# Kernel optimization log

Measured on AMD Instinct MI355X. Metric: run time of the kernel, lower is better.

## Reference

```python
import jax, jax.numpy as jnp
import numpy as np

NUM_SEG = 533  # ~ 400*400/300 superpixels from SLIC
C_FEAT = 2112
H = W = 400
SIM_THRESH = 0.97


def setup_inputs() -> dict:
    key = jax.random.key(0)
    ks = jax.random.split(key, 8)
    inp = {
        "feature_maps": jax.random.normal(ks[0], (C_FEAT, H, W), jnp.float32),
        "sp": jax.random.randint(ks[1], (H, W), 0, NUM_SEG, jnp.int32),
        "y": jax.random.randint(ks[2], (H, W), 0, 3, jnp.int32),
        "w1": jax.random.normal(ks[3], (C_FEAT, 1024), jnp.float32) * 0.02,
        "b1": jnp.zeros((1024,), jnp.float32),
        "w2": jax.random.normal(ks[4], (1024, 1024), jnp.float32) * 0.02,
        "b2": jnp.zeros((1024,), jnp.float32),
        "w3": jax.random.normal(ks[5], (1024, 32), jnp.float32) * 0.02,
        "b3": jnp.zeros((32,), jnp.float32),
        "wc": jax.random.normal(ks[6], (32, 2), jnp.float32) * 0.02,
        "bc": jnp.zeros((2,), jnp.float32),
    }
    return inp


def reference(feature_maps, sp, y, w1, b1, w2, b2, w3, b3, wc, bc):
    C = feature_maps.shape[0]
    feats = feature_maps.reshape(C, -1).T            # [HW, C]
    seg = sp.reshape(-1)                             # [HW]

    # fused per-superpixel gather + mean (replaces the per-segment Python loop)
    sums = jax.ops.segment_sum(feats, seg, num_segments=NUM_SEG)          # [S, C]
    cnts = jax.ops.segment_sum(jnp.ones_like(seg, dtype=feats.dtype), seg,
                               num_segments=NUM_SEG)                      # [S]
    mean_feat = sums / jnp.maximum(cnts, 1.0)[:, None]                    # [S, C]

    # per-superpixel majority label over classes {0,1,2}
    onehot = jax.nn.one_hot(y.reshape(-1), 3, dtype=jnp.float32)          # [HW, 3]
    counts = jax.ops.segment_sum(onehot, seg, num_segments=NUM_SEG)       # [S, 3]
    lab = jnp.argmax(counts, axis=1)                                      # first max, like torch
    ones_c, twos_c = counts[:, 1], counts[:, 2]
    tie_break = jnp.where(twos_c > ones_c, 2, jnp.where(ones_c > twos_c, 1, 0))
    lab = jnp.where(lab == 0, tie_break, lab)                             # [S]

    # batched MLP + classifier (replaces per-segment calls)
    h = jax.nn.relu(mean_feat @ w1 + b1)
    h = jax.nn.relu(h @ w2 + b2)
    h = jax.nn.relu(h @ w3 + b3)
    preds = jax.nn.softmax(h @ wc + bc, axis=-1)                          # [S, 2]

    # cosine-similarity kNN label propagation (matmul form of the O(n*m) loop)
    labeled = lab != 0
    det = jax.lax.stop_gradient(mean_feat)
    nrm = det / jnp.maximum(jnp.linalg.norm(det, axis=1, keepdims=True), 1e-12)
    aff = nrm @ nrm.T                                                     # [S, S]
    aff_masked = jnp.where(labeled[None, :], aff, -jnp.inf)               # cols: labeled only
    best = jnp.max(aff_masked, axis=1)
    best_idx = jnp.argmax(aff_masked, axis=1)
    propagate = (~labeled) & (best >= SIM_THRESH)
    new_lab = jnp.where(propagate, lab[best_idx], lab)                    # [S]

    return preds, lab, labeled, new_lab
```

## Files before the change

kernel.cpp:

```cpp
#include <hip/hip_runtime.h>
#include <math.h>

#define NSEG 533
#define CFEAT 2112
#define PIX 160000
#define SIM_THRESH 0.97f
#define RPG 1250
#define NCG 33
#define RTOT (RPG * NCG)
#define NBLK 256

typedef __attribute__((ext_vector_type(4))) float f32x4;
typedef __attribute__((ext_vector_type(4))) int   i32x4;
typedef __attribute__((ext_vector_type(8))) short bf16x8;

__device__ inline unsigned short f2bf_u16(float f) {
    unsigned u = __builtin_bit_cast(unsigned, f);
    return (unsigned short)((u + 0x7FFFu + ((u >> 16) & 1u)) >> 16);
}

__global__ __launch_bounds__(256) void k_counts(const int* __restrict__ sp,
                                                const int* __restrict__ y,
                                                int* __restrict__ c3) {
    __shared__ int h[NSEG * 3];
    for (int e = threadIdx.x; e < NSEG * 3; e += 256) h[e] = 0;
    __syncthreads();
    const int base = blockIdx.x * 5000;
    for (int p = threadIdx.x; p < 5000; p += 256) {
        int idx = base + p;
        atomicAdd(&h[sp[idx] * 3 + y[idx]], 1);
    }
    __syncthreads();
    for (int e = threadIdx.x; e < NSEG * 3; e += 256) {
        int v = h[e];
        if (v) atomicAdd(&c3[e], v);
    }
}

__global__ __launch_bounds__(256) void k_labels(const int* __restrict__ c3,
                                                int* __restrict__ lab,
                                                float* __restrict__ invc,
                                                float* __restrict__ out) {
    int s = blockIdx.x * 256 + threadIdx.x;
    if (s >= NSEG) return;
    int c0 = c3[s * 3 + 0], c1 = c3[s * 3 + 1], c2 = c3[s * 3 + 2];
    int cnt = c0 + c1 + c2;
    int idx = 0, best = c0;
    if (c1 > best) { best = c1; idx = 1; }
    if (c2 > best) { best = c2; idx = 2; }
    if (idx == 0) idx = (c2 > c1) ? 2 : ((c1 > c2) ? 1 : 0);
    lab[s] = idx;
    invc[s] = 1.0f / (float)(cnt > 0 ? cnt : 1);
    out[1066 + s] = (float)idx;
    out[1599 + s] = (idx != 0) ? 1.0f : 0.0f;
}

__global__ __launch_bounds__(1024, 4) void k_segsum_mfma(const float* __restrict__ fm,
                                                         const int* __restrict__ sp,
                                                         float* __restrict__ sums) {
    __shared__ char Bs[2][64 * 128];
    const int tid = threadIdx.x;
    const int lane = tid & 63, wave = tid >> 6;
    const int r = lane & 15, kg = lane >> 4;
    const int nmt = (wave < 2) ? 3 : 2;
    const int rswz = (r & 7) << 3;
    const int sch = tid >> 4;
    const int spx = tid & 15;
    const int wswz = (sch & 7) << 3;

    long long t0 = ((long long)blockIdx.x * RTOT) / NBLK;
    const long long t1 = ((long long)(blockIdx.x + 1) * RTOT) / NBLK;

    while (t0 < t1) {
        const int cg = (int)(t0 / RPG);
        const int r0 = (int)(t0 - (long long)cg * RPG);
        const long long cgend = (long long)(cg + 1) * RPG;
        const int rend = (int)(((t1 < cgend) ? t1 : cgend) - (long long)cg * RPG);
        const int c0 = cg * 64;
        const float* fmg = fm + (size_t)(c0 + sch) * PIX + spx * 8;

        f32x4 acc[3][4] = {};

        auto stage = [&](int rr) {
            const float* src = fmg + rr * 128;
            f32x4 u0 = *(const f32x4*)src;
            f32x4 u1 = *(const f32x4*)(src + 4);
            int w0 = __builtin_amdgcn_cvt_pk_fp8_f32(u0[0], u0[1], 0, false);
            w0 = __builtin_amdgcn_cvt_pk_fp8_f32(u0[2], u0[3], w0, true);
            int w1 = __builtin_amdgcn_cvt_pk_fp8_f32(u1[0], u1[1], 0, false);
            w1 = __builtin_amdgcn_cvt_pk_fp8_f32(u1[2], u1[3], w1, true);
            uint2 w = { (unsigned)w0, (unsigned)w1 };
            *(uint2*)(Bs[rr & 1] + sch * 128 + ((spx * 8) ^ wswz)) = w;
        };

        stage(r0);
        __syncthreads();

        for (int rr = r0; rr < rend; ++rr) {
            const bool pf = (rr + 1 < rend);
            f32x4 u0 = {}, u1 = {};
            if (pf) {
                const float* src = fmg + (rr + 1) * 128;
                u0 = *(const f32x4*)src;
                u1 = *(const f32x4*)(src + 4);
            }
            const char* bufc = Bs[rr & 1];
            const int* spr = sp + rr * 128 + kg * 8;
            i32x4 sa = *(const i32x4*)spr;
            i32x4 sb = *(const i32x4*)(spr + 4);

            #pragma unroll
            for (int ks = 0; ks < 4; ++ks) {
                i32x4 na, nb;
                if (ks < 3) {
                    na = *(const i32x4*)(spr + (ks + 1) * 32);
                    nb = *(const i32x4*)(spr + (ks + 1) * 32 + 4);
                }
                int seg[8] = { sa[0], sa[1], sa[2], sa[3], sb[0], sb[1], sb[2], sb[3] };
                uint2 vb[4];
                #pragma unroll
                for (int nt = 0; nt < 4; ++nt)
                    vb[nt] = *(const uint2*)(bufc + (nt * 16 + r) * 128 +
                                             ((ks * 32 + kg * 8) ^ rswz));
                #pragma unroll
                for (int i = 0; i < 3; ++i) {
                    if (i < nmt) {
                        const int tm = (i < 2) ? wave * 2 + i : 32 + wave;
                        const int tgt = tm * 16 + r;
                        unsigned a0 = ((seg[0] == tgt) ? 0x38u : 0u) |
                                      ((seg[1] == tgt) ? 0x3800u : 0u) |
                                      ((seg[2] == tgt) ? 0x380000u : 0u) |
                                      ((seg[3] == tgt) ? 0x38000000u : 0u);
                        unsigned a1 = ((seg[4] == tgt) ? 0x38u : 0u) |
                                      ((seg[5] == tgt) ? 0x3800u : 0u) |
                                      ((seg[6] == tgt) ? 0x380000u : 0u) |
                                      ((seg[7] == tgt) ? 0x3800u * 0x10000u : 0u);
                        if (__any((a0 | a1) != 0u)) {
                            long long av = __builtin_bit_cast(long long, (uint2){ a0, a1 });
                            acc[i][0] = __builtin_amdgcn_mfma_f32_16x16x32_fp8_fp8(
                                av, __builtin_bit_cast(long long, vb[0]), acc[i][0], 0, 0, 0);
                            acc[i][1] = __builtin_amdgcn_mfma_f32_16x16x32_fp8_fp8(
                                av, __builtin_bit_cast(long long, vb[1]), acc[i][1], 0, 0, 0);
                            acc[i][2] = __builtin_amdgcn_mfma_f32_16x16x32_fp8_fp8(
                                av, __builtin_bit_cast(long long, vb[2]), acc[i][2], 0, 0, 0);
                            acc[i][3] = __builtin_amdgcn_mfma_f32_16x16x32_fp8_fp8(
                                av, __builtin_bit_cast(long long, vb[3]), acc[i][3], 0, 0, 0);
                        }
                    }
                }
                if (ks < 3) { sa = na; sb = nb; }
            }

            if (pf) {
                int w0 = __builtin_amdgcn_cvt_pk_fp8_f32(u0[0], u0[1], 0, false);
                w0 = __builtin_amdgcn_cvt_pk_fp8_f32(u0[2], u0[3], w0, true);
                int w1 = __builtin_amdgcn_cvt_pk_fp8_f32(u1[0], u1[1], 0, false);
                w1 = __builtin_amdgcn_cvt_pk_fp8_f32(u1[2], u1[3], w1, true);
                uint2 w = { (unsigned)w0, (unsigned)w1 };
                *(uint2*)(Bs[(rr + 1) & 1] + sch * 128 + ((spx * 8) ^ wswz)) = w;
            }
            __syncthreads();
        }

        #pragma unroll
        for (int i = 0; i < 3; ++i) {
            if (i < nmt) {
                const int tm = (i < 2) ? wave * 2 + i : 32 + wave;
                #pragma unroll
                for (int nt = 0; nt < 4; ++nt) {
                    #pragma unroll
                    for (int q = 0; q < 4; ++q) {
                        int s = tm * 16 + kg * 4 + q;
                        unsafeAtomicAdd(&sums[(size_t)s * CFEAT + c0 + nt * 16 + r],
                                        acc[i][nt][q]);
                    }
                }
            }
        }
        t0 = (t1 < cgend) ? t1 : cgend;
        if (t0 < t1) __syncthreads();
    }
}

__global__ __launch_bounds__(256) void k_mean(float* __restrict__ feat,
                                              unsigned short* __restrict__ featbf,
                                              const float* __restrict__ invc,
                                              float* __restrict__ invn) {
    int s = blockIdx.x;
    float ic = invc[s];
    float ss = 0.0f;
    for (int c = threadIdx.x; c < CFEAT; c += 256) {
        float v = feat[(size_t)s * CFEAT + c] * ic;
        feat[(size_t)s * CFEAT + c] = v;
        featbf[(size_t)s * CFEAT + c] = f2bf_u16(v);
        ss += v * v;
    }
    __shared__ float red[256];
    red[threadIdx.x] = ss;
    __syncthreads();
    for (int st = 128; st > 0; st >>= 1) {
        if (threadIdx.x < st) red[threadIdx.x] += red[threadIdx.x + st];
        __syncthreads();
    }
    if (threadIdx.x == 0) invn[s] = 1.0f / fmaxf(sqrtf(red[0]), 1e-12f);
}

__global__ __launch_bounds__(256) void k_cvtT_all(const float* __restrict__ w1,
                                                  const float* __restrict__ w2,
                                                  const float* __restrict__ w3,
                                                  unsigned short* __restrict__ w1T,
                                                  unsigned short* __restrict__ w2T,
                                                  unsigned short* __restrict__ w3T) {
    const float* in; unsigned short* outT; int K, N, k0;
    int yb = blockIdx.y;
    if (yb < 66)       { in = w1; outT = w1T; K = CFEAT; N = 1024; k0 = yb * 32; }
    else if (yb < 98)  { in = w2; outT = w2T; K = 1024;  N = 1024; k0 = (yb - 66) * 32; }
    else               { in = w3; outT = w3T; K = 1024;  N = 32;   k0 = (yb - 98) * 32;
                         if (blockIdx.x != 0) return; }
    __shared__ float s[32][33];
    int n0 = blockIdx.x * 32;
    int lx = threadIdx.x & 31, ly = threadIdx.x >> 5;
    #pragma unroll
    for (int p = 0; p < 4; ++p)
        s[ly + p * 8][lx] = in[(size_t)(k0 + ly + p * 8) * N + n0 + lx];
    __syncthreads();
    #pragma unroll
    for (int p = 0; p < 4; ++p)
        outT[(size_t)(n0 + ly + p * 8) * K + k0 + lx] = f2bf_u16(s[lx][ly + p * 8]);
}

template <int RELU>
__global__ __launch_bounds__(256) void gemm_bf16(const unsigned short* __restrict__ A,
                                                 const unsigned short* __restrict__ Bt,
                                                 const float* __restrict__ bias,
                                                 float* __restrict__ Cf,
                                                 unsigned short* __restrict__ Cb,
                                                 int M, int N, int K) {
    __shared__ char As[64 * 128];
    __shared__ char Bs[64 * 128];
    const int tid = threadIdx.x;
    const int lane = tid & 63, wave = tid >> 6;
    const int r = lane & 15, kg = lane >> 4;
    const int m0 = blockIdx.y * 64, n0 = blockIdx.x * 64;
    const int row = tid >> 2, colw = tid & 3;
    const int swz = (row & 7) << 4;
    f32x4 acc[4] = {};

    for (int k0 = 0; k0 < K; k0 += 64) {
        {
            uint4 v0 = {}, v1 = {};
            if (m0 + row < M) {
                const unsigned short* src = A + (size_t)(m0 + row) * K + k0 + colw * 16;
                v0 = *(const uint4*)src;
                v1 = *(const uint4*)(src + 8);
            }
            *(uint4*)(As + row * 128 + ((colw * 32) ^ swz)) = v0;
            *(uint4*)(As + row * 128 + ((colw * 32 + 16) ^ swz)) = v1;
        }
        {
            uint4 v0 = {}, v1 = {};
            if (n0 + row < N) {
                const unsigned short* src = Bt + (size_t)(n0 + row) * K + k0 + colw * 16;
                v0 = *(const uint4*)src;
                v1 = *(const uint4*)(src + 8);
            }
            *(uint4*)(Bs + row * 128 + ((colw * 32) ^ swz)) = v0;
            *(uint4*)(Bs + row * 128 + ((colw * 32 + 16) ^ swz)) = v1;
        }
        __syncthreads();
        #pragma unroll
        for (int ks = 0; ks < 2; ++ks) {
            const int arow = wave * 16 + r;
            bf16x8 va = *(const bf16x8*)(As + arow * 128 + (((ks * 64) + kg * 16) ^ ((arow & 7) << 4)));
            #pragma unroll
            for (int nt = 0; nt < 4; ++nt) {
                const int brow = nt * 16 + r;
                bf16x8 vb = *(const bf16x8*)(Bs + brow * 128 + (((ks * 64) + kg * 16) ^ ((brow & 7) << 4)));
                acc[nt] = __builtin_amdgcn_mfma_f32_16x16x32_bf16(va, vb, acc[nt], 0, 0, 0);
            }
        }
        __syncthreads();
    }

    #pragma unroll
    for (int nt = 0; nt < 4; ++nt) {
        #pragma unroll
        for (int q = 0; q < 4; ++q) {
            int gr = m0 + wave * 16 + kg * 4 + q;
            int gc = n0 + nt * 16 + r;
            if (gr < M && gc < N) {
                float v = acc[nt][q];
                if (bias) v += bias[gc];
                if (RELU) v = fmaxf(v, 0.0f);
                if (Cf) Cf[(size_t)gr * N + gc] = v;
                if (Cb) Cb[(size_t)gr * N + gc] = f2bf_u16(v);
            }
        }
    }
}

__global__ __launch_bounds__(256) void k_prop(const float* __restrict__ aff,
                                              const int* __restrict__ lab,
                                              const float* __restrict__ invn,
                                              const float* __restrict__ h3,
                                              const float* __restrict__ wc,
                                              const float* __restrict__ bc,
                                              float* __restrict__ out) {
    int i = blockIdx.x;
    float invi = invn[i];
    float best = -INFINITY;
    int bidx = 0;
    for (int j = threadIdx.x; j < NSEG; j += 256) {
        if (lab[j] != 0) {
            float v = aff[(size_t)i * NSEG + j] * invi * invn[j];
            if (v > best) { best = v; bidx = j; }
        }
    }
    __shared__ float bv[256];
    __shared__ int bi[256];
    bv[threadIdx.x] = best;
    bi[threadIdx.x] = bidx;
    __syncthreads();
    for (int st = 128; st > 0; st >>= 1) {
        if (threadIdx.x < st) {
            float v2 = bv[threadIdx.x + st];
            int i2 = bi[threadIdx.x + st];
            if (v2 > bv[threadIdx.x] ||
                (v2 == bv[threadIdx.x] && i2 < bi[threadIdx.x])) {
                bv[threadIdx.x] = v2;
                bi[threadIdx.x] = i2;
            }
        }
        __syncthreads();
    }
    if (threadIdx.x == 0) {
        int li = lab[i];
        int nl = li;
        if (li == 0 && bv[0] >= SIM_THRESH) nl = lab[bi[0]];
        out[2132 + i] = (float)nl;
        float z0 = bc[0], z1 = bc[1];
        #pragma unroll
        for (int k = 0; k < 32; k++) {
            float h = h3[i * 32 + k];
            z0 += h * wc[k * 2 + 0];
            z1 += h * wc[k * 2 + 1];
        }
        float m = fmaxf(z0, z1);
        float e0 = expf(z0 - m), e1 = expf(z1 - m);
        float inv = 1.0f / (e0 + e1);
        out[i * 2 + 0] = e0 * inv;
        out[i * 2 + 1] = e1 * inv;
    }
}

extern "C" void kernel_launch(void* const* d_in, const int* in_sizes, int n_in,
                              void* d_out, int out_size, void* d_ws, size_t ws_size,
                              hipStream_t stream) {
    const float* fm = (const float*)d_in[0];
    const int* sp   = (const int*)d_in[1];
    const int* y    = (const int*)d_in[2];
    const float* w1 = (const float*)d_in[3];
    const float* b1 = (const float*)d_in[4];
    const float* w2 = (const float*)d_in[5];
    const float* b2 = (const float*)d_in[6];
    const float* w3 = (const float*)d_in[7];
    const float* b3 = (const float*)d_in[8];
    const float* wc = (const float*)d_in[9];
    const float* bc = (const float*)d_in[10];
    float* out = (float*)d_out;
    char* ws = (char*)d_ws;

    size_t off = 0;
    auto alloc = [&](size_t bytes) {
        size_t o = off;
        off += (bytes + 255) & ~(size_t)255;
        return o;
    };
    float*          feat   = (float*)(ws + alloc((size_t)544 * CFEAT * 4));
    unsigned short* featbf = (unsigned short*)(ws + alloc((size_t)544 * CFEAT * 2));
    unsigned short* w1T    = (unsigned short*)(ws + alloc((size_t)1024 * CFEAT * 2));
    unsigned short* w2T    = (unsigned short*)(ws + alloc((size_t)1024 * 1024 * 2));
    unsigned short* w3T    = (unsigned short*)(ws + alloc((size_t)32 * 1024 * 2));
    unsigned short* h1bf   = (unsigned short*)(ws + alloc((size_t)544 * 1024 * 2));
    unsigned short* h2bf   = (unsigned short*)(ws + alloc((size_t)544 * 1024 * 2));
    float*          h3     = (float*)(ws + alloc((size_t)544 * 32 * 4));
    float*          aff    = (float*)(ws + alloc((size_t)NSEG * NSEG * 4));
    int*            c3     = (int*)(ws + alloc((size_t)NSEG * 3 * 4));
    int*            lab    = (int*)(ws + alloc((size_t)NSEG * 4));
    float*          invc   = (float*)(ws + alloc((size_t)NSEG * 4));
    float*          invn   = (float*)(ws + alloc((size_t)NSEG * 4));

    hipMemsetAsync(feat, 0, (size_t)544 * CFEAT * 4, stream);
    hipMemsetAsync(c3, 0, (size_t)NSEG * 3 * 4, stream);

    k_cvtT_all<<<dim3(32, 130), 256, 0, stream>>>(w1, w2, w3, w1T, w2T, w3T);
    k_counts<<<32, 256, 0, stream>>>(sp, y, c3);
    k_labels<<<3, 256, 0, stream>>>(c3, lab, invc, out);
    k_segsum_mfma<<<NBLK, 1024, 0, stream>>>(fm, sp, feat);
    k_mean<<<NSEG, 256, 0, stream>>>(feat, featbf, invc, invn);

    gemm_bf16<1><<<dim3(16, 9), 256, 0, stream>>>(featbf, w1T, b1, nullptr, h1bf, NSEG, 1024, CFEAT);
    gemm_bf16<1><<<dim3(16, 9), 256, 0, stream>>>(h1bf, w2T, b2, nullptr, h2bf, NSEG, 1024, 1024);
    gemm_bf16<1><<<dim3(1, 9), 256, 0, stream>>>(h2bf, w3T, b3, h3, nullptr, NSEG, 32, 1024);
    gemm_bf16<0><<<dim3(9, 9), 256, 0, stream>>>(featbf, featbf, nullptr, aff, nullptr, NSEG, NSEG, CFEAT);

    k_prop<<<NSEG, 256, 0, stream>>>(aff, lab, invn, h3, wc, bc, out);
}
```

Measured before the change: 644.4 us.

## Use 16x16x128 scaled FP8 MFMA with 96-channel tiles in segment-sum kernel

```diff
diff --git a/kernel.cpp b/kernel.cpp
--- a/kernel.cpp
+++ b/kernel.cpp
@@ -6,12 +6,13 @@
 #define PIX 160000
 #define SIM_THRESH 0.97f
 #define RPG 1250
-#define NCG 33
+#define NCG 22
 #define RTOT (RPG * NCG)
 #define NBLK 256
 
 typedef __attribute__((ext_vector_type(4))) float f32x4;
 typedef __attribute__((ext_vector_type(4))) int   i32x4;
+typedef __attribute__((ext_vector_type(8))) int   i32x8;
 typedef __attribute__((ext_vector_type(8))) short bf16x8;
 
 __device__ inline unsigned short f2bf_u16(float f) {
@@ -58,15 +59,21 @@
 __global__ __launch_bounds__(1024, 4) void k_segsum_mfma(const float* __restrict__ fm,
                                                          const int* __restrict__ sp,
                                                          float* __restrict__ sums) {
-    __shared__ char Bs[2][64 * 128];
+    __shared__ char Bs[2][96 * 128];
     const int tid = threadIdx.x;
     const int lane = tid & 63, wave = tid >> 6;
     const int r = lane & 15, kg = lane >> 4;
-    const int nmt = (wave < 2) ? 3 : 2;
-    const int rswz = (r & 7) << 3;
-    const int sch = tid >> 4;
-    const int spx = tid & 15;
-    const int wswz = (sch & 7) << 3;
+    const int tgt0 = (wave * 2 + 0) * 16 + r;
+    const int tgt1 = (wave * 2 + 1) * 16 + r;
+    const bool tl = (wave < 12);
+    const int ttile = 32 + (wave >= 6 ? 1 : 0);
+    const int tnt = wave % 6;
+    const int tgtT = ttile * 16 + r;
+    const int rswz = (r & 7) << 4;
+    const int sch = tid >> 3;
+    const int spx = tid & 7;
+    const bool stg = (sch < 96);
+    const int wswz = (sch & 7) << 4;
 
     long long t0 = ((long long)blockIdx.x * RTOT) / NBLK;
     const long long t1 = ((long long)(blockIdx.x + 1) * RTOT) / NBLK;
@@ -76,105 +83,114 @@
         const int r0 = (int)(t0 - (long long)cg * RPG);
         const long long cgend = (long long)(cg + 1) * RPG;
         const int rend = (int)(((t1 < cgend) ? t1 : cgend) - (long long)cg * RPG);
-        const int c0 = cg * 64;
-        const float* fmg = fm + (size_t)(c0 + sch) * PIX + spx * 8;
-
-        f32x4 acc[3][4] = {};
-
-        auto stage = [&](int rr) {
-            const float* src = fmg + rr * 128;
-            f32x4 u0 = *(const f32x4*)src;
-            f32x4 u1 = *(const f32x4*)(src + 4);
-            int w0 = __builtin_amdgcn_cvt_pk_fp8_f32(u0[0], u0[1], 0, false);
-            w0 = __builtin_amdgcn_cvt_pk_fp8_f32(u0[2], u0[3], w0, true);
-            int w1 = __builtin_amdgcn_cvt_pk_fp8_f32(u1[0], u1[1], 0, false);
-            w1 = __builtin_amdgcn_cvt_pk_fp8_f32(u1[2], u1[3], w1, true);
-            uint2 w = { (unsigned)w0, (unsigned)w1 };
-            *(uint2*)(Bs[rr & 1] + sch * 128 + ((spx * 8) ^ wswz)) = w;
+        const int c0 = cg * 96;
+        const float* fmg = stg ? (fm + (size_t)(c0 + sch) * PIX + spx * 16) : fm;
+
+        f32x4 acc[13] = {};
+
+        auto cvtWrite = [&](int buf, f32x4 u0, f32x4 u1, f32x4 u2, f32x4 u3) {
+            if (!stg) return;
+            int a = __builtin_amdgcn_cvt_pk_fp8_f32(u0[0], u0[1], 0, false);
+            a = __builtin_amdgcn_cvt_pk_fp8_f32(u0[2], u0[3], a, true);
+            int b = __builtin_amdgcn_cvt_pk_fp8_f32(u1[0], u1[1], 0, false);
+            b = __builtin_amdgcn_cvt_pk_fp8_f32(u1[2], u1[3], b, true);
+            int c = __builtin_amdgcn_cvt_pk_fp8_f32(u2[0], u2[1], 0, false);
+            c = __builtin_amdgcn_cvt_pk_fp8_f32(u2[2], u2[3], c, true);
+            int d = __builtin_amdgcn_cvt_pk_fp8_f32(u3[0], u3[1], 0, false);
+            d = __builtin_amdgcn_cvt_pk_fp8_f32(u3[2], u3[3], d, true);
+            uint4 w = { (unsigned)a, (unsigned)b, (unsigned)c, (unsigned)d };
+            *(uint4*)(Bs[buf] + sch * 128 + ((spx * 16) ^ wswz)) = w;
         };
 
-        stage(r0);
+        {
+            f32x4 u0 = {}, u1 = {}, u2 = {}, u3 = {};
+            if (stg) {
+                const float* src = fmg + r0 * 128;
+                u0 = *(const f32x4*)src;
+                u1 = *(const f32x4*)(src + 4);
+                u2 = *(const f32x4*)(src + 8);
+                u3 = *(const f32x4*)(src + 12);
+            }
+            cvtWrite(r0 & 1, u0, u1, u2, u3);
+        }
         __syncthreads();
 
         for (int rr = r0; rr < rend; ++rr) {
             const bool pf = (rr + 1 < rend);
-            f32x4 u0 = {}, u1 = {};
-            if (pf) {
+            f32x4 u0 = {}, u1 = {}, u2 = {}, u3 = {};
+            if (pf && stg) {
                 const float* src = fmg + (rr + 1) * 128;
                 u0 = *(const f32x4*)src;
                 u1 = *(const f32x4*)(src + 4);
+                u2 = *(const f32x4*)(src + 8);
+                u3 = *(const f32x4*)(src + 12);
             }
             const char* bufc = Bs[rr & 1];
-            const int* spr = sp + rr * 128 + kg * 8;
-            i32x4 sa = *(const i32x4*)spr;
-            i32x4 sb = *(const i32x4*)(spr + 4);
-
+
+            unsigned aw0[8], aw1[8], awT[8];
+            const int* spr = sp + rr * 128 + kg * 32;
             #pragma unroll
-            for (int ks = 0; ks < 4; ++ks) {
-                i32x4 na, nb;
-                if (ks < 3) {
-                    na = *(const i32x4*)(spr + (ks + 1) * 32);
-                    nb = *(const i32x4*)(spr + (ks + 1) * 32 + 4);
+            for (int j = 0; j < 8; ++j) {
+                i32x4 s = *(const i32x4*)(spr + j * 4);
+                aw0[j] = ((s[0] == tgt0) ? 0x38u : 0u) |
+                         ((s[1] == tgt0) ? 0x3800u : 0u) |
+                         ((s[2] == tgt0) ? 0x380000u : 0u) |
+                         ((s[3] == tgt0) ? 0x38000000u : 0u);
+                aw1[j] = ((s[0] == tgt1) ? 0x38u : 0u) |
+                         ((s[1] == tgt1) ? 0x3800u : 0u) |
+                         ((s[2] == tgt1) ? 0x380000u : 0u) |
+                         ((s[3] == tgt1) ? 0x38000000u : 0u);
+                if (tl) {
+                    awT[j] = ((s[0] == tgtT) ? 0x38u : 0u) |
+                             ((s[1] == tgtT) ? 0x3800u : 0u) |
+                             ((s[2] == tgtT) ? 0x380000u : 0u) |
+                             ((s[3] == tgtT) ? 0x38000000u : 0u);
                 }
-                int seg[8] = { sa[0], sa[1], sa[2], sa[3], sb[0], sb[1], sb[2], sb[3] };
-                uint2 vb[4];
+            }
+            i32x8 va0 = __builtin_bit_cast(i32x8, aw0);
+            i32x8 va1 = __builtin_bit_cast(i32x8, aw1);
+
+            #pragma unroll
+            for (int nt = 0; nt < 6; ++nt) {
+                const int row = nt * 16 + r;
+                uint4 vbA = *(const uint4*)(bufc + row * 128 + ((kg * 32) ^ rswz));
+                uint4 vbB = *(const uint4*)(bufc + row * 128 + ((kg * 32 + 16) ^ rswz));
+                unsigned vbw[8] = { vbA.x, vbA.y, vbA.z, vbA.w, vbB.x, vbB.y, vbB.z, vbB.w };
+                i32x8 vb = __builtin_bit_cast(i32x8, vbw);
+                acc[nt] = __builtin_amdgcn_mfma_scale_f32_16x16x128_f8f6f4(
+                    va0, vb, acc[nt], 0, 0, 0, 0x7F7F7F7F, 0, 0x7F7F7F7F);
+                acc[6 + nt] = __builtin_amdgcn_mfma_scale_f32_16x16x128_f8f6f4(
+                    va1, vb, acc[6 + nt], 0, 0, 0, 0x7F7F7F7F, 0, 0x7F7F7F7F);
+                if (tl && nt == tnt) {
+                    i32x8 vaT = __builtin_bit_cast(i32x8, awT);
+                    acc[12] = __builtin_amdgcn_mfma_scale_f32_16x16x128_f8f6f4(
+                        vaT, vb, acc[12], 0, 0, 0, 0x7F7F7F7F, 0, 0x7F7F7F7F);
+                }
+            }
+
+            if (pf) cvtWrite((rr + 1) & 1, u0, u1, u2, u3);
+            __syncthreads();
+        }
+
+        #pragma unroll
+        for (int i = 0; i < 2; ++i) {
+            const int tm = wave * 2 + i;
+            #pragma unroll
+            for (int nt = 0; nt < 6; ++nt) {
                 #pragma unroll
-                for (int nt = 0; nt < 4; ++nt)
-                    vb[nt] = *(const uint2*)(bufc + (nt * 16 + r) * 128 +
-                                             ((ks * 32 + kg * 8) ^ rswz));
-                #pragma unroll
-                for (int i = 0; i < 3; ++i) {
-                    if (i < nmt) {
-                        const int tm = (i < 2) ? wave * 2 + i : 32 + wave;
-                        const int tgt = tm * 16 + r;
-                        unsigned a0 = ((seg[0] == tgt) ? 0x38u : 0u) |
-                                      ((seg[1] == tgt) ? 0x3800u : 0u) |
-                                      ((seg[2] == tgt) ? 0x380000u : 0u) |
-                                      ((seg[3] == tgt) ? 0x38000000u : 0u);
-                        unsigned a1 = ((seg[4] == tgt) ? 0x38u : 0u) |
-                                      ((seg[5] == tgt) ? 0x3800u : 0u) |
-                                      ((seg[6] == tgt) ? 0x380000u : 0u) |
-                                      ((seg[7] == tgt) ? 0x3800u * 0x10000u : 0u);
-                        if (__any((a0 | a1) != 0u)) {
-                            long long av = __builtin_bit_cast(long long, (uint2){ a0, a1 });
-                            acc[i][0] = __builtin_amdgcn_mfma_f32_16x16x32_fp8_fp8(
-                                av, __builtin_bit_cast(long long, vb[0]), acc[i][0], 0, 0, 0);
-                            acc[i][1] = __builtin_amdgcn_mfma_f32_16x16x32_fp8_fp8(
-                                av, __builtin_bit_cast(long long, vb[1]), acc[i][1], 0, 0, 0);
-                            acc[i][2] = __builtin_amdgcn_mfma_f32_16x16x32_fp8_fp8(
-                                av, __builtin_bit_cast(long long, vb[2]), acc[i][2], 0, 0, 0);
-                            acc[i][3] = __builtin_amdgcn_mfma_f32_16x16x32_fp8_fp8(
-                                av, __builtin_bit_cast(long long, vb[3]), acc[i][3], 0, 0, 0);
-                        }
-                    }
+                for (int q = 0; q < 4; ++q) {
+                    int s = tm * 16 + kg * 4 + q;
+                    unsafeAtomicAdd(&sums[(size_t)s * CFEAT + c0 + nt * 16 + r],
+                                    acc[i * 6 + nt][q]);
                 }
-                if (ks < 3) { sa = na; sb = nb; }
-            }
-
-            if (pf) {
-                int w0 = __builtin_amdgcn_cvt_pk_fp8_f32(u0[0], u0[1], 0, false);
-                w0 = __builtin_amdgcn_cvt_pk_fp8_f32(u0[2], u0[3], w0, true);
-                int w1 = __builtin_amdgcn_cvt_pk_fp8_f32(u1[0], u1[1], 0, false);
-                w1 = __builtin_amdgcn_cvt_pk_fp8_f32(u1[2], u1[3], w1, true);
-                uint2 w = { (unsigned)w0, (unsigned)w1 };
-                *(uint2*)(Bs[(rr + 1) & 1] + sch * 128 + ((spx * 8) ^ wswz)) = w;
-            }
-            __syncthreads();
-        }
-
-        #pragma unroll
-        for (int i = 0; i < 3; ++i) {
-            if (i < nmt) {
-                const int tm = (i < 2) ? wave * 2 + i : 32 + wave;
-                #pragma unroll
-                for (int nt = 0; nt < 4; ++nt) {
-                    #pragma unroll
-                    for (int q = 0; q < 4; ++q) {
-                        int s = tm * 16 + kg * 4 + q;
-                        unsafeAtomicAdd(&sums[(size_t)s * CFEAT + c0 + nt * 16 + r],
-                                        acc[i][nt][q]);
-                    }
-                }
+            }
+        }
+        if (tl) {
+            #pragma unroll
+            for (int q = 0; q < 4; ++q) {
+                int s = ttile * 16 + kg * 4 + q;
+                unsafeAtomicAdd(&sums[(size_t)s * CFEAT + c0 + tnt * 16 + r],
+                                acc[12][q]);
             }
         }
         t0 = (t1 < cgend) ? t1 : cgend;
```

New measurement: 1.073 ms. 66.6% more time.
